# Optimization experiments

Hardware: AMD Instinct MI355X
Metric: run time of the kernel (lower is better)

Reference implementation:

```python
import jax, jax.numpy as jnp
import numpy as np

EPS = 1e-12


def agnn_layer(x, row, col, num_nodes):
    """AGNN propagation with beta frozen at 1.0 (requires_grad=False in source).
    alpha_ij = softmax_{j in N(i)} ( beta * cos(x_i, x_j) ); out_i = sum_j alpha_ij * x_j.
    row = destination node of each edge (segment id), col = source node.
    """
    xn = x / (jnp.linalg.norm(x, axis=-1, keepdims=True) + EPS)  # unit-norm features
    score = jnp.sum(xn[row] * xn[col], axis=-1)                   # [E] beta=1 * cos sim
    smax = jax.ops.segment_max(score, row, num_segments=num_nodes)
    e = jnp.exp(score - smax[row])                                # stable softmax numerator
    denom = jax.ops.segment_sum(e, row, num_segments=num_nodes)
    alpha = e / jnp.maximum(denom[row], EPS)                      # [E]
    out = jax.ops.segment_sum(alpha[:, None] * x[col], row, num_segments=num_nodes)
    return out


def setup_inputs() -> dict:
    key = jax.random.key(0)
    ks = jax.random.split(key, 8)
    N, E = 100000, 1600000
    IN_DIM, HID, OUT_DIM = 128, 64, 64
    x = jax.random.normal(ks[0], (N, IN_DIM), dtype=jnp.float32)
    edge_row = jnp.sort(jax.random.randint(ks[1], (E,), 0, N))
    edge_col = jax.random.randint(ks[2], (E,), 0, N)
    # Linear params (PyTorch nn.Linear style: y = x @ W.T + b)
    s1 = 1.0 / np.sqrt(IN_DIM)
    W1 = jax.random.uniform(ks[3], (HID, IN_DIM), jnp.float32, -s1, s1)
    b1 = jax.random.uniform(ks[4], (HID,), jnp.float32, -s1, s1)
    s2 = 1.0 / np.sqrt(HID)
    W2 = jax.random.uniform(ks[5], (OUT_DIM, HID), jnp.float32, -s2, s2)
    b2 = jax.random.uniform(ks[6], (OUT_DIM,), jnp.float32, -s2, s2)
    return {"x": x, "edge_row": edge_row, "edge_col": edge_col,
            "W1": W1, "b1": b1, "W2": W2, "b2": b2}


def reference(x, edge_row, edge_col, W1, b1, W2, b2):
    N = x.shape[0]
    h = jax.nn.relu(x @ W1.T + b1)
    for _ in range(4):  # 4 frozen-beta AGNN layers
        h = jax.nn.relu(agnn_layer(h, edge_row, edge_col, N))
    return h @ W2.T + b2
```

## Files before the change

### kernel.cpp

```cpp
#include <hip/hip_runtime.h>


typedef _Float16 h2 __attribute__((ext_vector_type(2)));

union U4H { uint4 u; h2 h[4]; };
union U2H { uint2 u; h2 h[2]; };
union UHI { unsigned u; h2 h; };
union UF  { unsigned u; float f; int i; };

#define DEV_INLINE __device__ __forceinline__

DEV_INLINE h2 mkh2(float a, float b) {
    h2 r; r.x = (_Float16)a; r.y = (_Float16)b; return r;
}

template <int CTRL>
DEV_INLINE float dpp_addf(float x) {
    UF a, b;
    a.f = x;
    b.i = __builtin_amdgcn_update_dpp(0, a.i, CTRL, 0xF, 0xF, true);
    return x + b.f;
}

__global__ __launch_bounds__(256) void build_rowptr_scan(const int* __restrict__ row,
                                                         int* __restrict__ ptr,
                                                         int N, int E) {
    int e = blockIdx.x * blockDim.x + threadIdx.x;
    if (e >= E) return;
    const int r1 = row[e];
    const int r0 = (e == 0) ? -1 : row[e - 1];
    for (int i = r0 + 1; i <= r1; ++i) ptr[i] = e;
    if (e == E - 1) {
        for (int i = r1 + 1; i <= N; ++i) ptr[i] = E;
    }
}

#define PSEG 1024
__global__ __launch_bounds__(1024) void build_perm_seg(const int* __restrict__ ptr,
                                                       int* __restrict__ perm,
                                                       int N) {
    __shared__ int hist[256];
    __shared__ int tmp[256];
    const int t    = threadIdx.x;
    const int base = blockIdx.x * PSEG;
    const int end  = (base + PSEG < N) ? base + PSEG : N;
    const int cnt  = end - base;

    if (t < 256) hist[t] = 0;
    __syncthreads();

    int d = -1;
    if (t < cnt) {
        d = ptr[base + t + 1] - ptr[base + t];
        if (d > 255) d = 255;
        atomicAdd(&hist[d], 1);
    }
    __syncthreads();

    int h0 = (t < 256) ? hist[t] : 0;
    int* src = hist; int* dst = tmp;
    for (int off = 1; off < 256; off <<= 1) {
        if (t < 256) dst[t] = src[t] + (t >= off ? src[t - off] : 0);
        __syncthreads();
        int* tt = src; src = dst; dst = tt;
    }
    if (t < 256) src[t] -= h0;
    __syncthreads();

    if (t < cnt) {
        int pos = base + atomicAdd(&src[d], 1);
        perm[pos] = base + t;
    }
}

__global__ __launch_bounds__(512) void gemm1_relu(const float* __restrict__ x,
                                                  const float* __restrict__ W1,
                                                  const float* __restrict__ b1,
                                                  unsigned short* __restrict__ xn,
                                                  float* __restrict__ nrm,
                                                  int N) {
    __shared__ __align__(16) float Wt[32 * 64];
    __shared__ __align__(16) float xT[32 * 128];
    const int tid  = threadIdx.x;
    const int tx   = tid & 15;
    const int ty   = tid >> 4;
    const int base = blockIdx.x * 128;

    const float4* W4  = (const float4*)W1;
    const float4* x4p = (const float4*)x;

    const int wO  = tid & 63;
    const int wK4 = tid >> 6;
    const int mA  = tid & 127;
    const int kA  = tid >> 7;
    const int mB  = mA;
    const int kB  = kA + 4;
    const int nodeA = base + mA;

    float4 wv, xa_, xb_;
    wv = W4[wO * 32 + wK4];
    xa_ = make_float4(0.f, 0.f, 0.f, 0.f);
    xb_ = xa_;
    if (nodeA < N) {
        xa_ = x4p[(size_t)nodeA * 32 + kA];
        xb_ = x4p[(size_t)nodeA * 32 + kB];
    }

    float4 b4 = ((const float4*)b1)[tx];
    float4 acc[4];
    acc[0] = b4; acc[1] = b4; acc[2] = b4; acc[3] = b4;

    for (int c = 0; c < 4; ++c) {
        Wt[(4 * wK4 + 0) * 64 + wO] = wv.x;
        Wt[(4 * wK4 + 1) * 64 + wO] = wv.y;
        Wt[(4 * wK4 + 2) * 64 + wO] = wv.z;
        Wt[(4 * wK4 + 3) * 64 + wO] = wv.w;
        xT[(4 * kA + 0) * 128 + mA] = xa_.x;
        xT[(4 * kA + 1) * 128 + mA] = xa_.y;
        xT[(4 * kA + 2) * 128 + mA] = xa_.z;
        xT[(4 * kA + 3) * 128 + mA] = xa_.w;
        xT[(4 * kB + 0) * 128 + mB] = xb_.x;
        xT[(4 * kB + 1) * 128 + mB] = xb_.y;
        xT[(4 * kB + 2) * 128 + mB] = xb_.z;
        xT[(4 * kB + 3) * 128 + mB] = xb_.w;
        __syncthreads();

        if (c < 3) {
            const int ko = (c + 1) * 8;
            wv = W4[wO * 32 + ko + wK4];
            if (nodeA < N) {
                xa_ = x4p[(size_t)nodeA * 32 + ko + kA];
                xb_ = x4p[(size_t)nodeA * 32 + ko + kB];
            }
        }

#pragma unroll 4
        for (int k = 0; k < 32; ++k) {
            const float4 w4 = *(const float4*)&Wt[k * 64 + 4 * tx];
            const float4 xv = *(const float4*)&xT[k * 128 + 4 * ty];
            acc[0].x = fmaf(xv.x, w4.x, acc[0].x);
            acc[0].y = fmaf(xv.x, w4.y, acc[0].y);
            acc[0].z = fmaf(xv.x, w4.z, acc[0].z);
            acc[0].w = fmaf(xv.x, w4.w, acc[0].w);
            acc[1].x = fmaf(xv.y, w4.x, acc[1].x);
            acc[1].y = fmaf(xv.y, w4.y, acc[1].y);
            acc[1].z = fmaf(xv.y, w4.z, acc[1].z);
            acc[1].w = fmaf(xv.y, w4.w, acc[1].w);
            acc[2].x = fmaf(xv.z, w4.x, acc[2].x);
            acc[2].y = fmaf(xv.z, w4.y, acc[2].y);
            acc[2].z = fmaf(xv.z, w4.z, acc[2].z);
            acc[2].w = fmaf(xv.z, w4.w, acc[2].w);
            acc[3].x = fmaf(xv.w, w4.x, acc[3].x);
            acc[3].y = fmaf(xv.w, w4.y, acc[3].y);
            acc[3].z = fmaf(xv.w, w4.z, acc[3].z);
            acc[3].w = fmaf(xv.w, w4.w, acc[3].w);
        }
        if (c < 3) __syncthreads();
    }

#pragma unroll
    for (int mm = 0; mm < 4; ++mm) {
        float4 r = acc[mm];
        r.x = fmaxf(r.x, 0.f); r.y = fmaxf(r.y, 0.f);
        r.z = fmaxf(r.z, 0.f); r.w = fmaxf(r.w, 0.f);
        float s = fmaf(r.x, r.x, fmaf(r.y, r.y, fmaf(r.z, r.z, r.w * r.w)));
        s = dpp_addf<0xB1>(s);
        s = dpp_addf<0x4E>(s);
        s = dpp_addf<0x141>(s);
        s = dpp_addf<0x140>(s);
        const float nn  = sqrtf(s) + 1e-12f;
        const float inv = 1.f / nn;
        int node = base + 4 * ty + mm;
        if (node < N) {
            U2H pk;
            pk.h[0] = mkh2(r.x * inv, r.y * inv);
            pk.h[1] = mkh2(r.z * inv, r.w * inv);
            *(uint2*)&xn[(size_t)node * 64 + 4 * tx] = pk.u;
            if (tx == mm) nrm[node] = nn;
        }
    }
}

__global__ __launch_bounds__(256) void agnn_layer(const uint4* __restrict__ xn4,
                                                  const float* __restrict__ nrm,
                                                  const int* __restrict__ ptr,
                                                  const int* __restrict__ col,
                                                  const int* __restrict__ perm,
                                                  uint4* __restrict__ xo4,
                                                  float* __restrict__ nrmo,
                                                  int N) {
    const int tid  = threadIdx.x;
    const int lane = tid & 63;
    const int g    = (lane >> 3) & 1;
    const int sub  = lane & 7;
    const int slot = blockIdx.x * 16 + (tid >> 4);
    if (slot >= N) return;
    const int i = perm[slot];

    U4H hi_;
    hi_.u = xn4[(unsigned)i * 8u + sub];
    {
        const _Float16 L2E = (_Float16)1.4426950408889634f;
        h2 l2 = {L2E, L2E};
#pragma unroll
        for (int t = 0; t < 4; ++t) hi_.h[t] *= l2;
    }

    const int p0 = ptr[i], p1 = ptr[i + 1];

    float den = 0.f;
    U4H acc;
    acc.h[0] = mkh2(0.f, 0.f); acc.h[1] = mkh2(0.f, 0.f);
    acc.h[2] = mkh2(0.f, 0.f); acc.h[3] = mkh2(0.f, 0.f);

#define EDGE_BODY(VU, NRMJ)                                                  \
    {                                                                        \
        U4H xa; xa.u = (VU);                                                 \
        float sa = __builtin_amdgcn_fdot2(hi_.h[0], xa.h[0], 0.f, false);    \
        sa = __builtin_amdgcn_fdot2(hi_.h[1], xa.h[1], sa, false);           \
        float sb = __builtin_amdgcn_fdot2(hi_.h[2], xa.h[2], 0.f, false);    \
        sb = __builtin_amdgcn_fdot2(hi_.h[3], xa.h[3], sb, false);           \
        float s = sa + sb;                                                   \
        s = dpp_addf<0xB1>(s);                                               \
        s = dpp_addf<0x4E>(s);                                               \
        s = dpp_addf<0x141>(s);                                              \
        const float p = exp2f(s);                                            \
        den += p;                                                            \
        const _Float16 wh = (_Float16)(p * (NRMJ));                          \
        h2 w2 = {wh, wh};                                                    \
        acc.h[0] += w2 * xa.h[0];                                            \
        acc.h[1] += w2 * xa.h[1];                                            \
        acc.h[2] += w2 * xa.h[2];                                            \
        acc.h[3] += w2 * xa.h[3];                                            \
    }

    int e = p0 + g;
    for (; e + 2 < p1; e += 4) {
        const int ja = col[e];
        const int jb = col[e + 2];
        const uint4 va = xn4[(unsigned)ja * 8u + sub];
        const uint4 vb = xn4[(unsigned)jb * 8u + sub];
        const float na = nrm[ja];
        const float nb = nrm[jb];
        EDGE_BODY(va, na)
        EDGE_BODY(vb, nb)
    }
    if (e < p1) {
        const int j = col[e];
        const uint4 v = xn4[(unsigned)j * 8u + sub];
        const float nj = nrm[j];
        EDGE_BODY(v, nj)
    }
#undef EDGE_BODY

    {
        den = dpp_addf<0x140>(den);
#pragma unroll
        for (int t = 0; t < 4; ++t) {
            UHI a; a.h = acc.h[t];
            UHI b; b.u = (unsigned)__shfl_xor((int)a.u, 8, 64);
            acc.h[t] = a.h + b.h;
        }
    }

    const float id = 1.f / fmaxf(den, 1e-12f);
    float o[8];
#pragma unroll
    for (int t = 0; t < 4; ++t) {
        o[2 * t]     = fmaxf((float)acc.h[t].x * id, 0.f);
        o[2 * t + 1] = fmaxf((float)acc.h[t].y * id, 0.f);
    }

    float s2 = 0.f;
#pragma unroll
    for (int t = 0; t < 8; ++t) s2 = fmaf(o[t], o[t], s2);
    s2 = dpp_addf<0xB1>(s2);
    s2 = dpp_addf<0x4E>(s2);
    s2 = dpp_addf<0x141>(s2);
    const float nn  = sqrtf(s2) + 1e-12f;
    const float inv = 1.f / nn;

    if (g == 0) {
        U4H ov;
        ov.h[0] = mkh2(o[0] * inv, o[1] * inv);
        ov.h[1] = mkh2(o[2] * inv, o[3] * inv);
        ov.h[2] = mkh2(o[4] * inv, o[5] * inv);
        ov.h[3] = mkh2(o[6] * inv, o[7] * inv);
        xo4[(unsigned)i * 8u + sub] = ov.u;
        if (sub == 0) nrmo[i] = nn;
    }
}

__global__ __launch_bounds__(512) void gemm2(const unsigned short* __restrict__ xn,
                                             const float* __restrict__ nrm,
                                             const float* __restrict__ W2,
                                             const float* __restrict__ b2,
                                             float* __restrict__ out,
                                             int N) {
    __shared__ __align__(16) float Wt[64 * 64];
    __shared__ __align__(16) float xT[64 * 128];
    const int tid  = threadIdx.x;
    const int tx   = tid & 15;
    const int ty   = tid >> 4;
    const int base = blockIdx.x * 128;

    {
        const float4* W4 = (const float4*)W2;
#pragma unroll
        for (int it = 0; it < 2; ++it) {
            int idx = tid + it * 512;
            int o = idx & 63, k4 = idx >> 6;
            float4 v = W4[o * 16 + k4];
            Wt[(4 * k4 + 0) * 64 + o] = v.x;
            Wt[(4 * k4 + 1) * 64 + o] = v.y;
            Wt[(4 * k4 + 2) * 64 + o] = v.z;
            Wt[(4 * k4 + 3) * 64 + o] = v.w;
        }
        const uint2* x2 = (const uint2*)xn;
#pragma unroll
        for (int it = 0; it < 4; ++it) {
            int idx = tid + it * 512;
            int mm = idx & 127, k4 = idx >> 7;
            int node = base + mm;
            U2H v; v.u = make_uint2(0u, 0u);
            float nn = 0.f;
            if (node < N) { v.u = x2[(size_t)node * 16 + k4]; nn = nrm[node]; }
            xT[(4 * k4 + 0) * 128 + mm] = (float)v.h[0].x * nn;
            xT[(4 * k4 + 1) * 128 + mm] = (float)v.h[0].y * nn;
            xT[(4 * k4 + 2) * 128 + mm] = (float)v.h[1].x * nn;
            xT[(4 * k4 + 3) * 128 + mm] = (float)v.h[1].y * nn;
        }
    }
    __syncthreads();

    float4 b4 = ((const float4*)b2)[tx];
    float4 acc[4];
    acc[0] = b4; acc[1] = b4; acc[2] = b4; acc[3] = b4;

#pragma unroll 4
    for (int k = 0; k < 64; ++k) {
        const float4 w4 = *(const float4*)&Wt[k * 64 + 4 * tx];
        const float4 xv = *(const float4*)&xT[k * 128 + 4 * ty];
        acc[0].x = fmaf(xv.x, w4.x, acc[0].x);
        acc[0].y = fmaf(xv.x, w4.y, acc[0].y);
        acc[0].z = fmaf(xv.x, w4.z, acc[0].z);
        acc[0].w = fmaf(xv.x, w4.w, acc[0].w);
        acc[1].x = fmaf(xv.y, w4.x, acc[1].x);
        acc[1].y = fmaf(xv.y, w4.y, acc[1].y);
        acc[1].z = fmaf(xv.y, w4.z, acc[1].z);
        acc[1].w = fmaf(xv.y, w4.w, acc[1].w);
        acc[2].x = fmaf(xv.z, w4.x, acc[2].x);
        acc[2].y = fmaf(xv.z, w4.y, acc[2].y);
        acc[2].z = fmaf(xv.z, w4.z, acc[2].z);
        acc[2].w = fmaf(xv.z, w4.w, acc[2].w);
        acc[3].x = fmaf(xv.w, w4.x, acc[3].x);
        acc[3].y = fmaf(xv.w, w4.y, acc[3].y);
        acc[3].z = fmaf(xv.w, w4.z, acc[3].z);
        acc[3].w = fmaf(xv.w, w4.w, acc[3].w);
    }

#pragma unroll
    for (int mm = 0; mm < 4; ++mm) {
        int node = base + 4 * ty + mm;
        if (node < N) *(float4*)&out[(size_t)node * 64 + 4 * tx] = acc[mm];
    }
}

extern "C" void kernel_launch(void* const* d_in, const int* in_sizes, int n_in,
                              void* d_out, int out_size, void* d_ws, size_t ws_size,
                              hipStream_t stream) {
    const float* x   = (const float*)d_in[0];
    const int*   row = (const int*)d_in[1];
    const int*   col = (const int*)d_in[2];
    const float* W1  = (const float*)d_in[3];
    const float* b1  = (const float*)d_in[4];
    const float* W2  = (const float*)d_in[5];
    const float* b2  = (const float*)d_in[6];
    float* out = (float*)d_out;

    const int N = in_sizes[0] / 128;
    const int E = in_sizes[1];

    char* ws = (char*)d_ws;
    size_t off = 0;
    unsigned short* ha = (unsigned short*)(ws + off); off += (size_t)N * 64 * 2;
    unsigned short* hb = (unsigned short*)(ws + off); off += (size_t)N * 64 * 2;
    float* na_  = (float*)(ws + off); off += (size_t)N * sizeof(float);
    float* nb_  = (float*)(ws + off); off += (size_t)N * sizeof(float);
    int*   ptr  = (int*)  (ws + off); off += (size_t)(N + 1) * sizeof(int);
    off = (off + 15) & ~(size_t)15;
    int*   perm = (int*)  (ws + off); off += (size_t)N * sizeof(int);
    (void)ws_size; (void)n_in; (void)out_size;

    build_rowptr_scan<<<(E + 255) / 256, 256, 0, stream>>>(row, ptr, N, E);

    build_perm_seg<<<(N + PSEG - 1) / PSEG, 1024, 0, stream>>>(ptr, perm, N);

    const int nbG = (N + 127) / 128;
    gemm1_relu<<<nbG, 512, 0, stream>>>(x, W1, b1, ha, na_, N);

    const int nb16 = (N + 15) / 16;
    unsigned short* hc = ha; unsigned short* hn = hb;
    float* nc = na_; float* nn = nb_;
    for (int l = 0; l < 4; ++l) {
        agnn_layer<<<nb16, 256, 0, stream>>>((const uint4*)hc, nc, ptr, col, perm,
                                             (uint4*)hn, nn, N);
        unsigned short* t = hc; hc = hn; hn = t;
        float* tf = nc; nc = nn; nn = tf;
    }

    gemm2<<<nbG, 512, 0, stream>>>(hc, nc, W2, b2, out, N);
}
```

Baseline: 298.2 us.

## Batch eight neighbor gathers per iteration and pack node metadata into int4

The permutation kernel now stores node id and row pointer bounds together as an int4, so each AGNN slot gets its edge range in one load instead of chasing perm then ptr. The edge loop splits each node's edges into two contiguous halves, one per half-group, and issues eight col, feature and norm loads before any compute, which raises memory-level parallelism on the gathers. Tail lanes clamp their index and mask the weight to zero. A launch-bounds occupancy hint of 6 is added. The cost is more registers per thread and wasted masked work on low-degree nodes, since the average degree is about 16, so each half handles about 8 edges.

```diff
diff --git a/kernel.cpp b/kernel.cpp
--- a/kernel.cpp
+++ b/kernel.cpp
@@ -37,7 +37,7 @@
 
 #define PSEG 1024
 __global__ __launch_bounds__(1024) void build_perm_seg(const int* __restrict__ ptr,
-                                                       int* __restrict__ perm,
+                                                       int4* __restrict__ meta,
                                                        int N) {
     __shared__ int hist[256];
     __shared__ int tmp[256];
@@ -49,9 +49,11 @@
     if (t < 256) hist[t] = 0;
     __syncthreads();
 
-    int d = -1;
+    int d = -1, p0v = 0, p1v = 0;
     if (t < cnt) {
-        d = ptr[base + t + 1] - ptr[base + t];
+        p0v = ptr[base + t];
+        p1v = ptr[base + t + 1];
+        d = p1v - p0v;
         if (d > 255) d = 255;
         atomicAdd(&hist[d], 1);
     }
@@ -69,7 +71,7 @@
 
     if (t < cnt) {
         int pos = base + atomicAdd(&src[d], 1);
-        perm[pos] = base + t;
+        meta[pos] = make_int4(base + t, p0v, p1v, 0);
     }
 }
 
@@ -181,21 +183,23 @@
     }
 }
 
-__global__ __launch_bounds__(256) void agnn_layer(const uint4* __restrict__ xn4,
-                                                  const float* __restrict__ nrm,
-                                                  const int* __restrict__ ptr,
-                                                  const int* __restrict__ col,
-                                                  const int* __restrict__ perm,
-                                                  uint4* __restrict__ xo4,
-                                                  float* __restrict__ nrmo,
-                                                  int N) {
+__global__ __launch_bounds__(256, 6) void agnn_layer(const uint4* __restrict__ xn4,
+                                                     const float* __restrict__ nrm,
+                                                     const int4* __restrict__ meta,
+                                                     const int* __restrict__ col,
+                                                     uint4* __restrict__ xo4,
+                                                     float* __restrict__ nrmo,
+                                                     int N) {
     const int tid  = threadIdx.x;
     const int lane = tid & 63;
     const int g    = (lane >> 3) & 1;
     const int sub  = lane & 7;
     const int slot = blockIdx.x * 16 + (tid >> 4);
     if (slot >= N) return;
-    const int i = perm[slot];
+
+    const int4 m0 = meta[slot];
+    const int i  = m0.x;
+    const int p0 = m0.y, p1 = m0.z;
 
     U4H hi_;
     hi_.u = xn4[(unsigned)i * 8u + sub];
@@ -203,77 +207,76 @@
         const _Float16 L2E = (_Float16)1.4426950408889634f;
         h2 l2 = {L2E, L2E};
 #pragma unroll
-        for (int t = 0; t < 4; ++t) hi_.h[t] *= l2;
-    }
-
-    const int p0 = ptr[i], p1 = ptr[i + 1];
+        for (int c = 0; c < 4; ++c) hi_.h[c] *= l2;
+    }
+
+    const int mid = p0 + ((p1 - p0 + 1) >> 1);
+    int       t   = g ? mid : p0;
+    const int e_  = g ? p1  : mid;
 
     float den = 0.f;
     U4H acc;
     acc.h[0] = mkh2(0.f, 0.f); acc.h[1] = mkh2(0.f, 0.f);
     acc.h[2] = mkh2(0.f, 0.f); acc.h[3] = mkh2(0.f, 0.f);
 
-#define EDGE_BODY(VU, NRMJ)                                                  \
-    {                                                                        \
-        U4H xa; xa.u = (VU);                                                 \
-        float sa = __builtin_amdgcn_fdot2(hi_.h[0], xa.h[0], 0.f, false);    \
-        sa = __builtin_amdgcn_fdot2(hi_.h[1], xa.h[1], sa, false);           \
-        float sb = __builtin_amdgcn_fdot2(hi_.h[2], xa.h[2], 0.f, false);    \
-        sb = __builtin_amdgcn_fdot2(hi_.h[3], xa.h[3], sb, false);           \
-        float s = sa + sb;                                                   \
-        s = dpp_addf<0xB1>(s);                                               \
-        s = dpp_addf<0x4E>(s);                                               \
-        s = dpp_addf<0x141>(s);                                              \
-        const float p = exp2f(s);                                            \
-        den += p;                                                            \
-        const _Float16 wh = (_Float16)(p * (NRMJ));                          \
-        h2 w2 = {wh, wh};                                                    \
-        acc.h[0] += w2 * xa.h[0];                                            \
-        acc.h[1] += w2 * xa.h[1];                                            \
-        acc.h[2] += w2 * xa.h[2];                                            \
-        acc.h[3] += w2 * xa.h[3];                                            \
-    }
-
-    int e = p0 + g;
-    for (; e + 2 < p1; e += 4) {
-        const int ja = col[e];
-        const int jb = col[e + 2];
-        const uint4 va = xn4[(unsigned)ja * 8u + sub];
-        const uint4 vb = xn4[(unsigned)jb * 8u + sub];
-        const float na = nrm[ja];
-        const float nb = nrm[jb];
-        EDGE_BODY(va, na)
-        EDGE_BODY(vb, nb)
-    }
-    if (e < p1) {
-        const int j = col[e];
-        const uint4 v = xn4[(unsigned)j * 8u + sub];
-        const float nj = nrm[j];
-        EDGE_BODY(v, nj)
-    }
-#undef EDGE_BODY
-
-    {
-        den = dpp_addf<0x140>(den);
-#pragma unroll
-        for (int t = 0; t < 4; ++t) {
-            UHI a; a.h = acc.h[t];
-            UHI b; b.u = (unsigned)__shfl_xor((int)a.u, 8, 64);
-            acc.h[t] = a.h + b.h;
-        }
+    for (; t < e_; t += 8) {
+        const int nb = e_ - t;
+        int   jj[8];
+        uint4 v[8];
+        float nm[8];
+
+#pragma unroll
+        for (int k = 0; k < 8; ++k) {
+            int e = t + k;
+            e = (e < e_) ? e : (e_ - 1);
+            jj[k] = col[e];
+        }
+#pragma unroll
+        for (int k = 0; k < 8; ++k) v[k] = xn4[(unsigned)jj[k] * 8u + sub];
+#pragma unroll
+        for (int k = 0; k < 8; ++k) nm[k] = nrm[jj[k]];
+
+#pragma unroll
+        for (int k = 0; k < 8; ++k) {
+            U4H xa; xa.u = v[k];
+            float sa = __builtin_amdgcn_fdot2(hi_.h[0], xa.h[0], 0.f, false);
+            sa = __builtin_amdgcn_fdot2(hi_.h[1], xa.h[1], sa, false);
+            float sb = __builtin_amdgcn_fdot2(hi_.h[2], xa.h[2], 0.f, false);
+            sb = __builtin_amdgcn_fdot2(hi_.h[3], xa.h[3], sb, false);
+            float s = sa + sb;
+            s = dpp_addf<0xB1>(s);
+            s = dpp_addf<0x4E>(s);
+            s = dpp_addf<0x141>(s);
+            const float p = (k < nb) ? exp2f(s) : 0.f;
+            den += p;
+            const _Float16 wh = (_Float16)(p * nm[k]);
+            h2 w2 = {wh, wh};
+            acc.h[0] += w2 * xa.h[0];
+            acc.h[1] += w2 * xa.h[1];
+            acc.h[2] += w2 * xa.h[2];
+            acc.h[3] += w2 * xa.h[3];
+        }
+    }
+
+    den = dpp_addf<0x140>(den);
+#pragma unroll
+    for (int c = 0; c < 4; ++c) {
+        UHI a; a.h = acc.h[c];
+        UHI b; b.u = (unsigned)__shfl_xor((int)a.u, 8, 64);
+        acc.h[c] = a.h + b.h;
     }
 
     const float id = 1.f / fmaxf(den, 1e-12f);
     float o[8];
 #pragma unroll
-    for (int t = 0; t < 4; ++t) {
-        o[2 * t]     = fmaxf((float)acc.h[t].x * id, 0.f);
-        o[2 * t + 1] = fmaxf((float)acc.h[t].y * id, 0.f);
+    for (int c = 0; c < 4; ++c) {
+        o[2 * c]     = fmaxf((float)acc.h[c].x * id, 0.f);
+        o[2 * c + 1] = fmaxf((float)acc.h[c].y * id, 0.f);
     }
 
     float s2 = 0.f;
 #pragma unroll
-    for (int t = 0; t < 8; ++t) s2 = fmaf(o[t], o[t], s2);
+    for (int c = 0; c < 8; ++c) s2 = fmaf(o[c], o[c], s2);
     s2 = dpp_addf<0xB1>(s2);
     s2 = dpp_addf<0x4E>(s2);
     s2 = dpp_addf<0x141>(s2);
@@ -389,12 +392,12 @@
     float* nb_  = (float*)(ws + off); off += (size_t)N * sizeof(float);
     int*   ptr  = (int*)  (ws + off); off += (size_t)(N + 1) * sizeof(int);
     off = (off + 15) & ~(size_t)15;
-    int*   perm = (int*)  (ws + off); off += (size_t)N * sizeof(int);
+    int4*  meta = (int4*) (ws + off); off += (size_t)N * sizeof(int4);
     (void)ws_size; (void)n_in; (void)out_size;
 
     build_rowptr_scan<<<(E + 255) / 256, 256, 0, stream>>>(row, ptr, N, E);
 
-    build_perm_seg<<<(N + PSEG - 1) / PSEG, 1024, 0, stream>>>(ptr, perm, N);
+    build_perm_seg<<<(N + PSEG - 1) / PSEG, 1024, 0, stream>>>(ptr, meta, N);
 
     const int nbG = (N + 127) / 128;
     gemm1_relu<<<nbG, 512, 0, stream>>>(x, W1, b1, ha, na_, N);
@@ -403,7 +406,7 @@
     unsigned short* hc = ha; unsigned short* hn = hb;
     float* nc = na_; float* nn = nb_;
     for (int l = 0; l < 4; ++l) {
-        agnn_layer<<<nb16, 256, 0, stream>>>((const uint4*)hc, nc, ptr, col, perm,
+        agnn_layer<<<nb16, 256, 0, stream>>>((const uint4*)hc, nc, meta, col,
                                              (uint4*)hn, nn, N);
         unsigned short* t = hc; hc = hn; hn = t;
         float* tf = nc; nc = nn; nn = tf;
```

Result: no change. 296.7 us (-0.5%).
